# Performance work log

Hardware: AMD Instinct MI355X
Metric: run time of the kernel (lower is better)

## Reference

```python
import jax, jax.numpy as jnp
import numpy as np

NEG_INF = -1e30


def setup_inputs() -> dict:
    key = jax.random.key(0)
    kx, km, kq, kk, kv, ko = jax.random.split(key, 6)
    B, D, L = 2, 1024, 2048
    H, DK = 16, 64
    x = jax.random.normal(kx, (B, D, L), dtype=jnp.float32)
    mask = (jax.random.uniform(km, (B, L)) < 0.9).astype(jnp.float32)
    # per-head projection weights, stacked: (H, D, DK); output proj (D, H*DK)==(D, D)
    sq = 1.0 / np.sqrt(D)
    Wq = jax.random.normal(kq, (H, D, DK), dtype=jnp.float32) * sq
    Wk = jax.random.normal(kk, (H, D, DK), dtype=jnp.float32) * sq
    Wv = jax.random.normal(kv, (H, D, DK), dtype=jnp.float32) * sq
    Wo = jax.random.normal(ko, (D, H * DK), dtype=jnp.float32) * sq
    return {"x": x, "mask": mask, "Wq": Wq, "Wk": Wk, "Wv": Wv, "Wo": Wo}


def reference(x, mask, Wq, Wk, Wv, Wo):
    # x: (B, D, L); original transposes to (B, L, D)
    B, D, L = x.shape
    H, _, DK = Wq.shape
    xt = jnp.transpose(x, (0, 2, 1))  # (B, L, D)
    q = jnp.einsum('bld,hdk->bhlk', xt, Wq)
    k = jnp.einsum('bld,hdk->bhlk', xt, Wk)
    v = jnp.einsum('bld,hdk->bhlk', xt, Wv)
    scores = jnp.einsum('bhlk,bhmk->bhlm', q, k) * (1.0 / np.sqrt(DK))
    # masked log-softmax over keys (hmask), squad-style: mask*logit + (1-mask)*-1e30
    hmask = mask[:, None, None, :]  # (B,1,1,Lk)
    masked = hmask * scores + (1.0 - hmask) * NEG_INF
    logp = jax.nn.log_softmax(masked, axis=-1)
    # second softmax over the log-probs, then multiplicative vmask on query dim
    p = jax.nn.softmax(logp, axis=-1) * mask[:, None, :, None]
    heads = jnp.einsum('bhlm,bhmk->bhlk', p, v)  # (B,H,L,DK)
    head = jnp.transpose(heads, (0, 2, 1, 3)).reshape(B, L, H * DK)
    out = jnp.einsum('ble,de->bld', head, Wo)  # matmul(head, Wo) with Wo (D, H*DK)... 
    # NOTE: torch.matmul(head, Wo) treats Wo as (H*DK_in, D_out) only if square; here
    # Wo is (D, H*DK) with D == H*DK, and torch contracts head's last dim with Wo's FIRST dim:
    out = head @ Wo  # (B, L, H*DK) @ (D, H*DK) requires D==H*DK; contracts dim 0 of Wo
    return jnp.transpose(out, (0, 2, 1))  # (B, D, L)


if __name__ == "__main__":
    print(reference(**setup_inputs()).shape)
```

## Files before the change

kernel.cpp:

```cpp
#include <hip/hip_runtime.h>
#include <hip/hip_bf16.h>

typedef unsigned short u16;
typedef unsigned int u32;
typedef unsigned long long u64;
typedef short s8v __attribute__((ext_vector_type(8)));
typedef short s4v __attribute__((ext_vector_type(4)));
typedef __bf16 bfv8 __attribute__((ext_vector_type(8)));
typedef float f4 __attribute__((ext_vector_type(4)));

static constexpr int B = 2, D = 1024, L = 2048, H = 16, DK = 64, E = 1024;
static constexpr float QSCALE = 0.125f * 1.44269504088896340736f;
static constexpr float SMB = -16.0f;
static constexpr float MASKB = -12000.0f;

#define DEV __device__ __forceinline__

DEV u16 f2bf(float f) {
  unsigned int u = __float_as_uint(f);
  u += 0x7FFFu + ((u >> 16) & 1u);
  return (u16)(u >> 16);
}
DEV float fexp2(float x) { return __builtin_amdgcn_exp2f(x); }
DEV u32 pkbf(float a, float b) {
  __hip_bfloat162 h = __float22bfloat162_rn(float2{a, b});
  u32 r;
  __builtin_memcpy(&r, &h, 4);
  return r;
}

DEV f4 mfma16(s4v a, s4v b, f4 c) {
  return __builtin_amdgcn_mfma_f32_16x16x16bf16_1k(a, b, c, 0, 0, 0);
}

#define GLD_LDS16(gp, lp)                                                     \
  __builtin_amdgcn_global_load_lds(                                           \
      (const __attribute__((address_space(1))) void*)(gp),                    \
      (__attribute__((address_space(3))) void*)(lp), 16, 0, 0)

__global__ __launch_bounds__(256) void k_prep(
    const float* __restrict__ x, const float* __restrict__ Wq,
    const float* __restrict__ Wk, const float* __restrict__ Wv,
    const float* __restrict__ Wo, u16* __restrict__ xt, u16* __restrict__ Wt,
    u16* __restrict__ WoT) {
  __shared__ u16 t[64][67];
  const int tid = threadIdx.x;
  const int g = blockIdx.x;
  const float* src;
  u16* dst;
  int sld, dld;
  if (g < 1024) {
    const int b = g >> 9, dt = (g >> 5) & 15, lt = g & 31;
    src = x + ((size_t)b * D + dt * 64) * L + lt * 64;
    sld = L;
    dst = xt + ((size_t)b * L + lt * 64) * D + dt * 64;
    dld = D;
  } else if (g < 1792) {
    const int u = g - 1024;
    const int w = u >> 8, h = (u >> 4) & 15, dt = u & 15;
    const float* Ws = (w == 0) ? Wq : ((w == 1) ? Wk : Wv);
    src = Ws + ((size_t)h * D + dt * 64) * DK;
    sld = DK;
    dst = Wt + ((size_t)(w * H + h) * DK) * D + dt * 64;
    dld = D;
  } else {
    const int v = g - 1792;
    const int et = v >> 4, dt = v & 15;
    src = Wo + ((size_t)et * 64) * D + dt * 64;
    sld = D;
    dst = WoT + ((size_t)dt * 64) * E + et * 64;
    dld = E;
  }
  const int r = tid >> 2, c16 = (tid & 3) * 16;
#pragma unroll
  for (int j = 0; j < 16; j += 4) {
    const f4 v4 = *(const f4*)(src + (size_t)r * sld + c16 + j);
    t[r][c16 + j]     = f2bf(v4[0]);
    t[r][c16 + j + 1] = f2bf(v4[1]);
    t[r][c16 + j + 2] = f2bf(v4[2]);
    t[r][c16 + j + 3] = f2bf(v4[3]);
  }
  __syncthreads();
  s8v o0, o1;
#pragma unroll
  for (int i = 0; i < 8; ++i) {
    o0[i] = (short)t[c16 + i][r];
    o1[i] = (short)t[c16 + 8 + i][r];
  }
  *(s8v*)(dst + (size_t)r * dld + c16)     = o0;
  *(s8v*)(dst + (size_t)r * dld + c16 + 8) = o1;
}

template <int AR>
DEV void gemm_tile(const u16* __restrict__ A, const u16* __restrict__ Bt,
                   int arow0, int brow0, u16* As, u16* Bs,
                   f4 (&acc)[AR / 32][4]) {
  const int tid = threadIdx.x;
  const int wid = tid >> 6, lane = tid & 63;
  const int q = lane >> 4, ln = lane & 15;
  const int wr = wid >> 1, wc = wid & 1;
  const int lrow = lane >> 3;
  const int lc = (lane & 7) ^ lrow;
  const int f0 = (q ^ (ln & 7)) * 8;
  const int f1 = ((q + 4) ^ (ln & 7)) * 8;
  constexpr int MT = AR / 32;

  for (int k0 = 0; k0 < 1024; k0 += 64) {
    __syncthreads();
#pragma unroll
    for (int j = 0; j < AR / 32; ++j) {
      const int rb = wid * (AR / 4) + j * 8;
      GLD_LDS16(A + (size_t)(arow0 + rb + lrow) * 1024 + k0 + lc * 8,
                As + rb * 64);
    }
#pragma unroll
    for (int j = 0; j < 4; ++j) {
      const int rb = wid * 32 + j * 8;
      GLD_LDS16(Bt + (size_t)(brow0 + rb + lrow) * 1024 + k0 + lc * 8,
                Bs + rb * 64);
    }
    __syncthreads();
#pragma unroll
    for (int ks = 0; ks < 2; ++ks) {
      const int fc = ks ? f1 : f0;
      bfv8 af[MT], bf[4];
#pragma unroll
      for (int mt = 0; mt < MT; ++mt)
        af[mt] = *(const bfv8*)(As + (wr * (AR / 2) + mt * 16 + ln) * 64 + fc);
#pragma unroll
      for (int nt = 0; nt < 4; ++nt)
        bf[nt] = *(const bfv8*)(Bs + (wc * 64 + nt * 16 + ln) * 64 + fc);
#pragma unroll
      for (int mt = 0; mt < MT; ++mt)
#pragma unroll
        for (int nt = 0; nt < 4; ++nt)
          acc[mt][nt] = __builtin_amdgcn_mfma_f32_16x16x32_bf16(
              af[mt], bf[nt], acc[mt][nt], 0, 0, 0);
    }
  }
}

__global__ __launch_bounds__(256, 3) void k_qkvg(
    const u16* __restrict__ xt, const u16* __restrict__ Wt,
    u16* __restrict__ Q, u16* __restrict__ K, u16* __restrict__ Vt) {
  __shared__ u16 As[128 * 64];
  __shared__ u16 Bs[128 * 64];
  const int bm = blockIdx.x, bn = blockIdx.y;
  f4 acc[4][4];
#pragma unroll
  for (int mt = 0; mt < 4; ++mt)
#pragma unroll
    for (int nt = 0; nt < 4; ++nt) acc[mt][nt] = (f4){0.f, 0.f, 0.f, 0.f};
  gemm_tile<128>(xt, Wt, bm * 128, bn * 128, As, Bs, acc);

  const int tid = threadIdx.x, wid = tid >> 6, lane = tid & 63;
  const int q = lane >> 4, ln = lane & 15;
  const int wr = wid >> 1, wc = wid & 1;
  const int h2 = bn * 2 + wc;
  const int wsel = h2 >> 4, h = h2 & 15;
  const int b = bm >> 4;
  const int lbase = (bm & 15) * 128 + wr * 64;
  if (wsel == 0) {
    u16* dst = Q + (size_t)(b * H + h) * L * DK;
#pragma unroll
    for (int mt = 0; mt < 4; ++mt)
#pragma unroll
      for (int nt = 0; nt < 4; ++nt)
#pragma unroll
        for (int r = 0; r < 4; ++r)
          dst[(size_t)(lbase + mt * 16 + q * 4 + r) * DK + nt * 16 + ln] =
              f2bf(acc[mt][nt][r] * QSCALE);
  } else if (wsel == 1) {
    u16* dst = K + (size_t)(b * H + h) * L * DK;
#pragma unroll
    for (int mt = 0; mt < 4; ++mt)
#pragma unroll
      for (int nt = 0; nt < 4; ++nt)
#pragma unroll
        for (int r = 0; r < 4; ++r)
          dst[(size_t)(lbase + mt * 16 + q * 4 + r) * DK + nt * 16 + ln] =
              f2bf(acc[mt][nt][r]);
  } else {
    u16* dst = Vt + (size_t)(b * H + h) * DK * L;
#pragma unroll
    for (int mt = 0; mt < 4; ++mt)
#pragma unroll
      for (int nt = 0; nt < 4; ++nt) {
        const u64 pk = (u64)pkbf(acc[mt][nt][0], acc[mt][nt][1]) |
                       ((u64)pkbf(acc[mt][nt][2], acc[mt][nt][3]) << 32);
        *(u64*)(dst + (size_t)(nt * 16 + ln) * L + lbase + mt * 16 + q * 4) =
            pk;
      }
  }
}

__global__ __launch_bounds__(256, 2) void k_attn(
    const u16* __restrict__ Q, const u16* __restrict__ K,
    const u16* __restrict__ Vt, const float* __restrict__ mask,
    u16* __restrict__ Hd) {
  __shared__ u16 kt[2][128 * 64];
  __shared__ u16 vt[2][2][64 * 64];
  __shared__ __align__(16) float mb[L];
  const int h = blockIdx.x, lt = blockIdx.y, b = blockIdx.z;
  const int tid = threadIdx.x;
  const int w = tid >> 6, lane = tid & 63, q = lane >> 4, ln = lane & 15;
  for (int i = tid; i < L; i += 256)
    mb[i] = (mask[(size_t)b * L + i] != 0.0f) ? SMB : MASKB;

  const int bh = b * H + h;
  const u16* Qp = Q + (size_t)bh * L * DK;
  const u16* Kp = K + (size_t)bh * L * DK;
  const u16* Vp = Vt + (size_t)bh * DK * L;
  const int lq = lt * 128 + w * 32;

  bfv8 qf[2][2];
#pragma unroll
  for (int mt = 0; mt < 2; ++mt) {
    qf[mt][0] = *(const bfv8*)(Qp + (size_t)(lq + mt * 16 + ln) * DK + q * 8);
    qf[mt][1] =
        *(const bfv8*)(Qp + (size_t)(lq + mt * 16 + ln) * DK + 32 + q * 8);
  }

  const int lrow = lane >> 3;
  const int lc = (lane & 7) ^ lrow;
  const int fr0 = w * 16 + lrow, fr1 = fr0 + 8;
  const int c0 = (q ^ (ln & 7)) * 8;
  const int c1 = ((q + 4) ^ (ln & 7)) * 8;

  auto stage = [&](int m0, int bufi) {
#pragma unroll
    for (int j = 0; j < 4; ++j) {
      const int rb = w * 32 + j * 8;
      GLD_LDS16(Kp + (size_t)(m0 + rb + lrow) * DK + lc * 8,
                &kt[bufi][rb * 64]);
    }
#pragma unroll
    for (int kh = 0; kh < 2; ++kh) {
      GLD_LDS16(Vp + (size_t)fr0 * L + m0 + kh * 64 + lc * 8,
                &vt[bufi][kh][(w * 16) * 64]);
      GLD_LDS16(Vp + (size_t)fr1 * L + m0 + kh * 64 + lc * 8,
                &vt[bufi][kh][(w * 16 + 8) * 64]);
    }
  };

  f4 ot[2][4];
#pragma unroll
  for (int mt = 0; mt < 2; ++mt)
#pragma unroll
    for (int i = 0; i < 4; ++i) ot[mt][i] = (f4){0.f, 0.f, 0.f, 0.f};
  float lp[2] = {0.f, 0.f};

  stage(0, 0);
  for (int it = 0; it < L / 128; ++it) {
    const int m0 = it * 128;
    __syncthreads();
    if (it + 1 < L / 128) stage(m0 + 128, (it + 1) & 1);
    const int cur = it & 1;
    const u16* ktc = &kt[cur][0];

    s4v pb[2][8];
#pragma unroll
    for (int nt = 0; nt < 8; ++nt) {
      const int krow = nt * 16 + ln;
      const bfv8 kf0 = *(const bfv8*)(ktc + krow * 64 + c0);
      const bfv8 kf1 = *(const bfv8*)(ktc + krow * 64 + c1);
      const f4 mbv = *(const f4*)(mb + m0 + nt * 16 + q * 4);
#pragma unroll
      for (int mt = 0; mt < 2; ++mt) {
        f4 a = mbv;
        a = __builtin_amdgcn_mfma_f32_16x16x32_bf16(kf0, qf[mt][0], a, 0, 0,
                                                    0);
        a = __builtin_amdgcn_mfma_f32_16x16x32_bf16(kf1, qf[mt][1], a, 0, 0,
                                                    0);
        const float p0 = fexp2(a[0]);
        const float p1 = fexp2(a[1]);
        const float p2 = fexp2(a[2]);
        const float p3 = fexp2(a[3]);
        lp[mt] += (p0 + p1) + (p2 + p3);
        const u64 pk = (u64)pkbf(p0, p1) | ((u64)pkbf(p2, p3) << 32);
        pb[mt][nt] = __builtin_bit_cast(s4v, pk);
      }
    }
#pragma unroll
    for (int kh = 0; kh < 2; ++kh) {
      const u16* vtc = &vt[cur][kh][0];
#pragma unroll
      for (int dt = 0; dt < 4; ++dt) {
        const int vrow = dt * 16 + ln;
        const int vbase = vrow * 64 + (q & 1) * 4;
        const int rx = vrow & 7;
        s4v av[4];
#pragma unroll
        for (int kc = 0; kc < 4; ++kc)
          av[kc] =
              *(const s4v*)(vtc + vbase + (((kc * 2 + (q >> 1)) ^ rx) * 8));
#pragma unroll
        for (int kc = 0; kc < 4; ++kc)
#pragma unroll
          for (int mt = 0; mt < 2; ++mt)
            ot[mt][dt] = mfma16(av[kc], pb[mt][kh * 4 + kc], ot[mt][dt]);
      }
    }
  }
#pragma unroll
  for (int mt = 0; mt < 2; ++mt) {
    lp[mt] += __shfl_xor(lp[mt], 16);
    lp[mt] += __shfl_xor(lp[mt], 32);
    const float linv =
        (mb[lq + mt * 16 + ln] > -100.0f) ? (1.0f / lp[mt]) : 0.0f;
#pragma unroll
    for (int dt = 0; dt < 4; ++dt) {
      const u64 pk =
          (u64)pkbf(ot[mt][dt][0] * linv, ot[mt][dt][1] * linv) |
          ((u64)pkbf(ot[mt][dt][2] * linv, ot[mt][dt][3] * linv) << 32);
      *(u64*)(Hd + (size_t)(b * L + lq + mt * 16 + ln) * E + h * DK + dt * 16 +
              q * 4) = pk;
    }
  }
}

__global__ __launch_bounds__(256, 2) void k_projg(const u16* __restrict__ WoT,
                                                  const u16* __restrict__ Hd,
                                                  float* __restrict__ out) {
  __shared__ u16 As[64 * 64];
  __shared__ u16 Bs[128 * 64];
  const int bm = blockIdx.x, bn = blockIdx.y;
  f4 acc[2][4];
#pragma unroll
  for (int mt = 0; mt < 2; ++mt)
#pragma unroll
    for (int nt = 0; nt < 4; ++nt) acc[mt][nt] = (f4){0.f, 0.f, 0.f, 0.f};
  gemm_tile<64>(WoT, Hd, bm * 64, bn * 128, As, Bs, acc);

  const int tid = threadIdx.x, wid = tid >> 6, lane = tid & 63;
  const int q = lane >> 4, ln = lane & 15;
  const int wr = wid >> 1, wc = wid & 1;
#pragma unroll
  for (int mt = 0; mt < 2; ++mt)
#pragma unroll
    for (int nt = 0; nt < 4; ++nt)
#pragma unroll
      for (int r = 0; r < 4; ++r) {
        const int d = bm * 64 + wr * 32 + mt * 16 + q * 4 + r;
        const int n = bn * 128 + wc * 64 + nt * 16 + ln;
        const int bb = n >> 11, l = n & 2047;
        out[((size_t)(bb * D + d)) * L + l] = acc[mt][nt][r];
      }
}

extern "C" void kernel_launch(void* const* d_in, const int* in_sizes, int n_in,
                              void* d_out, int out_size, void* d_ws,
                              size_t ws_size, hipStream_t stream) {
  const float* x    = (const float*)d_in[0];
  const float* mask = (const float*)d_in[1];
  const float* Wq   = (const float*)d_in[2];
  const float* Wk   = (const float*)d_in[3];
  const float* Wv   = (const float*)d_in[4];
  const float* Wo   = (const float*)d_in[5];
  u16* ws = (u16*)d_ws;
  u16* Qws  = ws;
  u16* Kws  = ws + 4194304;
  u16* Vtws = ws + 8388608;
  u16* WoTw = ws + 12582912;
  u16* Wtws = ws + 13631488;
  u16* xtws = ws + 16777216;
  u16* Hdws = ws + 16777216;

  k_prep<<<2048, 256, 0, stream>>>(x, Wq, Wk, Wv, Wo, xtws, Wtws, WoTw);
  k_qkvg<<<dim3(32, 24), 256, 0, stream>>>(xtws, Wtws, Qws, Kws, Vtws);
  k_attn<<<dim3(16, 16, 2), 256, 0, stream>>>(Qws, Kws, Vtws, mask, Hdws);
  k_projg<<<dim3(16, 32), 256, 0, stream>>>(WoTw, Hdws, (float*)d_out);
}
```

Measured before the change: 180.9 us.

## Cut attention LDS footprint to fit three blocks per CU

Removes the per-block LDS mask bias array and single-buffers the V tile, so V is loaded during the score phase and consumed after a second barrier. The mask is read directly from global memory and converted to the exp2 bias in registers. This lowers shared memory use so launch bounds can request three resident blocks per CU instead of two. The cost is an extra __syncthreads per tile, less prefetch distance for V, and global mask loads in the inner loop.

```diff
diff --git a/kernel.cpp b/kernel.cpp
--- a/kernel.cpp
+++ b/kernel.cpp
@@ -194,23 +194,21 @@
   }
 }
 
-__global__ __launch_bounds__(256, 2) void k_attn(
+__global__ __launch_bounds__(256, 3) void k_attn(
     const u16* __restrict__ Q, const u16* __restrict__ K,
     const u16* __restrict__ Vt, const float* __restrict__ mask,
     u16* __restrict__ Hd) {
   __shared__ u16 kt[2][128 * 64];
-  __shared__ u16 vt[2][2][64 * 64];
-  __shared__ __align__(16) float mb[L];
+  __shared__ u16 vt[2][64 * 64];
   const int h = blockIdx.x, lt = blockIdx.y, b = blockIdx.z;
   const int tid = threadIdx.x;
   const int w = tid >> 6, lane = tid & 63, q = lane >> 4, ln = lane & 15;
-  for (int i = tid; i < L; i += 256)
-    mb[i] = (mask[(size_t)b * L + i] != 0.0f) ? SMB : MASKB;
 
   const int bh = b * H + h;
   const u16* Qp = Q + (size_t)bh * L * DK;
   const u16* Kp = K + (size_t)bh * L * DK;
   const u16* Vp = Vt + (size_t)bh * DK * L;
+  const float* mp = mask + (size_t)b * L;
   const int lq = lt * 128 + w * 32;
 
   bfv8 qf[2][2];
@@ -227,19 +225,21 @@
   const int c0 = (q ^ (ln & 7)) * 8;
   const int c1 = ((q + 4) ^ (ln & 7)) * 8;
 
-  auto stage = [&](int m0, int bufi) {
+  auto stageK = [&](int m0, int bufi) {
 #pragma unroll
     for (int j = 0; j < 4; ++j) {
       const int rb = w * 32 + j * 8;
       GLD_LDS16(Kp + (size_t)(m0 + rb + lrow) * DK + lc * 8,
                 &kt[bufi][rb * 64]);
     }
+  };
+  auto stageV = [&](int m0) {
 #pragma unroll
     for (int kh = 0; kh < 2; ++kh) {
       GLD_LDS16(Vp + (size_t)fr0 * L + m0 + kh * 64 + lc * 8,
-                &vt[bufi][kh][(w * 16) * 64]);
+                &vt[kh][(w * 16) * 64]);
       GLD_LDS16(Vp + (size_t)fr1 * L + m0 + kh * 64 + lc * 8,
-                &vt[bufi][kh][(w * 16 + 8) * 64]);
+                &vt[kh][(w * 16 + 8) * 64]);
     }
   };
 
@@ -250,13 +250,13 @@
     for (int i = 0; i < 4; ++i) ot[mt][i] = (f4){0.f, 0.f, 0.f, 0.f};
   float lp[2] = {0.f, 0.f};
 
-  stage(0, 0);
+  stageK(0, 0);
   for (int it = 0; it < L / 128; ++it) {
     const int m0 = it * 128;
     __syncthreads();
-    if (it + 1 < L / 128) stage(m0 + 128, (it + 1) & 1);
-    const int cur = it & 1;
-    const u16* ktc = &kt[cur][0];
+    stageV(m0);
+    if (it + 1 < L / 128) stageK(m0 + 128, (it + 1) & 1);
+    const u16* ktc = &kt[it & 1][0];
 
     s4v pb[2][8];
 #pragma unroll
@@ -264,7 +264,10 @@
       const int krow = nt * 16 + ln;
       const bfv8 kf0 = *(const bfv8*)(ktc + krow * 64 + c0);
       const bfv8 kf1 = *(const bfv8*)(ktc + krow * 64 + c1);
-      const f4 mbv = *(const f4*)(mb + m0 + nt * 16 + q * 4);
+      const f4 m4 = *(const f4*)(mp + m0 + nt * 16 + q * 4);
+      f4 mbv;
+#pragma unroll
+      for (int i = 0; i < 4; ++i) mbv[i] = (m4[i] != 0.0f) ? SMB : MASKB;
 #pragma unroll
       for (int mt = 0; mt < 2; ++mt) {
         f4 a = mbv;
@@ -281,9 +284,11 @@
         pb[mt][nt] = __builtin_bit_cast(s4v, pk);
       }
     }
+    __syncthreads();
+
 #pragma unroll
     for (int kh = 0; kh < 2; ++kh) {
-      const u16* vtc = &vt[cur][kh][0];
+      const u16* vtc = &vt[kh][0];
 #pragma unroll
       for (int dt = 0; dt < 4; ++dt) {
         const int vrow = dt * 16 + ln;
@@ -306,8 +311,8 @@
   for (int mt = 0; mt < 2; ++mt) {
     lp[mt] += __shfl_xor(lp[mt], 16);
     lp[mt] += __shfl_xor(lp[mt], 32);
-    const float linv =
-        (mb[lq + mt * 16 + ln] > -100.0f) ? (1.0f / lp[mt]) : 0.0f;
+    const float qm = mp[lq + mt * 16 + ln];
+    const float linv = (qm != 0.0f) ? (1.0f / lp[mt]) : 0.0f;
 #pragma unroll
     for (int dt = 0; dt < 4; ++dt) {
       const u64 pk =
```

Result: slower. 214.6 us (+18.7%).
